# Optimization experiments

Measured on AMD Instinct MI355X. Metric: run time of the kernel, lower is better.

The kernel has to match this reference:

```python
import jax, jax.numpy as jnp
import numpy as np

B, N1, N2, D = 2, 512, 512, 128


def setup_inputs() -> dict:
    key = jax.random.key(0)
    ks = jax.random.split(key, 7)
    return {
        "x0": jax.random.normal(ks[0], (B, N1, D), dtype=jnp.float32),
        "x": jax.random.normal(ks[1], (B, N1, D), dtype=jnp.float32),
        "y": jax.random.normal(ks[2], (B, N2, D), dtype=jnp.float32),
        "W1": jax.random.normal(ks[3], (3 * D, D), dtype=jnp.float32) * (1.0 / np.sqrt(3 * D)),
        "b1": jax.random.normal(ks[4], (D,), dtype=jnp.float32) * 0.02,
        "W2": jax.random.normal(ks[5], (D, 1), dtype=jnp.float32) * (1.0 / np.sqrt(D)),
        "b2": jax.random.normal(ks[6], (1,), dtype=jnp.float32) * 0.02,
    }


def reference(x0, x, y, W1, b1, W2, b2):
    # linear1(concat([x0, x, y], -1)) == x0 @ W1[:D] + x @ W1[D:2D] + y @ W1[2D:] + b1
    d = x.shape[-1]
    Wa, Wb, Wc = W1[:d], W1[d:2 * d], W1[2 * d:]
    # small GEMMs on the un-expanded operands, then broadcast-add over the pair grid
    hx = jnp.einsum('bnd,de->bne', x0, Wa) + jnp.einsum('bnd,de->bne', x, Wb)  # [b, n1, d]
    hy = jnp.einsum('bmd,de->bme', y, Wc)                                      # [b, n2, d]
    h = hx[:, :, None, :] + hy[:, None, :, :] + b1                             # [b, n1, n2, d]
    h = jax.nn.gelu(h, approximate=False)                                      # torch nn.GELU default (erf)
    o = jnp.einsum('bnme,eo->bnmo', h, W2) + b2                                # [b, n1, n2, 1]
    return o[..., 0]                                                           # [b, n1, n2]
```

## Files before the change

kernel.cpp:

```cpp
#include <hip/hip_runtime.h>

#define BB 2
#define NN1 512
#define NN2 512
#define DD 128
#define TS 16
#define SXPAD 132

typedef float v4f __attribute__((ext_vector_type(4)));

struct GeluPoly {
    float p[10];
    constexpr GeluPoly() : p{} {
        const int N = 10;
        const double PI = 3.14159265358979323846;
        double fv[10] = {};
        double xv[10] = {};
        for (int j = 0; j < N; ++j) {
            double th = PI * (j + 0.5) / N;
            double cth = 1.0, term = 1.0, t2 = th * th;
            for (int k = 1; k <= 30; ++k) {
                term *= -t2 / ((2.0 * k - 1.0) * (2.0 * k));
                cth += term;
            }
            xv[j] = cth;
            double t = 4.5 * (cth + 1.0);
            double s = t > 1.0 ? t : 1.0;
            for (int it = 0; it < 64; ++it) s = 0.5 * (s + t / s);
            double x = s * 0.70710678118654752440;
            double esum = 0.0, pw = x, fact = 1.0;
            for (int k = 0; k < 48; ++k) {
                if (k > 0) { fact *= (double)k; pw *= x * x; }
                double tk = pw / (fact * (2.0 * k + 1.0));
                esum += (k & 1) ? -tk : tk;
            }
            double erfv = 1.12837916709551257390 * esum;
            fv[j] = 0.5 * erfv / s;
        }
        double ck[10] = {};
        for (int k = 0; k < N; ++k) {
            double sum = 0.0;
            for (int j = 0; j < N; ++j) {
                double Tk = 1.0;
                if (k >= 1) {
                    double Tm2 = 1.0, Tm1 = xv[j];
                    Tk = xv[j];
                    for (int i = 2; i <= k; ++i) {
                        Tk = 2.0 * xv[j] * Tm1 - Tm2;
                        Tm2 = Tm1; Tm1 = Tk;
                    }
                }
                sum += fv[j] * Tk;
            }
            ck[k] = 2.0 * sum / N;
        }
        ck[0] *= 0.5;
        double T[10][10] = {};
        T[0][0] = 1.0;
        T[1][1] = 1.0;
        for (int k = 2; k < N; ++k)
            for (int i = 0; i < N; ++i)
                T[k][i] = 2.0 * (i > 0 ? T[k - 1][i - 1] : 0.0) - T[k - 2][i];
        double pd[10] = {};
        for (int k = 0; k < N; ++k)
            for (int i = 0; i < N; ++i)
                pd[i] += ck[k] * T[k][i];
        for (int i = 0; i < N; ++i) p[i] = (float)pd[i];
    }
};
static constexpr GeluPoly GP{};

__device__ __forceinline__ float gelu_poly(float s) {
    float c = __builtin_amdgcn_fmed3f(s, -3.0f, 3.0f);
    float t = c * c;
    float u = __builtin_fmaf(t, 0.22222222222222222f, -1.0f);
    float q = GP.p[9];
    #pragma unroll
    for (int k = 8; k >= 0; --k) q = __builtin_fmaf(q, u, GP.p[k]);
    return s * __builtin_fmaf(c, q, 0.5f);
}

#define PR 8
__global__ __launch_bounds__(256) void proj_kernel(
    const float* __restrict__ x0, const float* __restrict__ x,
    const float* __restrict__ y,  const float* __restrict__ W1,
    const float* __restrict__ b1, float* __restrict__ hx, float* __restrict__ hy) {
    const int e = threadIdx.x & (DD - 1);
    const int g = threadIdx.x >> 7;
    const int nxb = (BB * NN1) / PR;
    const float* Wa = W1;
    const float* Wb = W1 + DD * DD;
    const float* Wc = W1 + 2 * DD * DD;

    if (blockIdx.x < nxb) {
        const int row0 = blockIdx.x * PR + g * (PR / 2);
        float acc0 = b1[e], acc1 = b1[e], acc2 = b1[e], acc3 = b1[e];
        #pragma unroll 4
        for (int d = 0; d < DD; ++d) {
            const float wa = Wa[d * DD + e];
            const float wb = Wb[d * DD + e];
            acc0 += x0[(row0 + 0) * DD + d] * wa + x[(row0 + 0) * DD + d] * wb;
            acc1 += x0[(row0 + 1) * DD + d] * wa + x[(row0 + 1) * DD + d] * wb;
            acc2 += x0[(row0 + 2) * DD + d] * wa + x[(row0 + 2) * DD + d] * wb;
            acc3 += x0[(row0 + 3) * DD + d] * wa + x[(row0 + 3) * DD + d] * wb;
        }
        hx[(row0 + 0) * DD + e] = acc0;
        hx[(row0 + 1) * DD + e] = acc1;
        hx[(row0 + 2) * DD + e] = acc2;
        hx[(row0 + 3) * DD + e] = acc3;
    } else {
        const int row0 = (blockIdx.x - nxb) * PR + g * (PR / 2);
        float acc0 = 0.f, acc1 = 0.f, acc2 = 0.f, acc3 = 0.f;
        #pragma unroll 4
        for (int d = 0; d < DD; ++d) {
            const float wc = Wc[d * DD + e];
            acc0 += y[(row0 + 0) * DD + d] * wc;
            acc1 += y[(row0 + 1) * DD + d] * wc;
            acc2 += y[(row0 + 2) * DD + d] * wc;
            acc3 += y[(row0 + 3) * DD + d] * wc;
        }
        hy[(row0 + 0) * DD + e] = acc0;
        hy[(row0 + 1) * DD + e] = acc1;
        hy[(row0 + 2) * DD + e] = acc2;
        hy[(row0 + 3) * DD + e] = acc3;
    }
}

__global__ __launch_bounds__(256) void cross_kernel(
    const float* __restrict__ hx, const float* __restrict__ hy,
    const float* __restrict__ W2, const float* __restrict__ b2,
    float* __restrict__ out) {
    __shared__ float sx[TS][SXPAD];
    __shared__ float sy[TS][SXPAD];
    __shared__ float sw[DD];

    const int b  = blockIdx.z;
    const int n0 = blockIdx.y * TS;
    const int m0 = blockIdx.x * TS;
    const int tid = threadIdx.x;

    for (int i = tid; i < TS * (DD / 4); i += 256) {
        const int r  = i >> 5;
        const int c4 = i & 31;
        *(v4f*)&sx[r][c4 * 4] =
            *(const v4f*)&hx[((b * NN1) + n0 + r) * DD + c4 * 4];
        *(v4f*)&sy[r][c4 * 4] =
            *(const v4f*)&hy[((b * NN2) + m0 + r) * DD + c4 * 4];
    }
    if (tid < DD) sw[tid] = W2[tid];
    __syncthreads();

    const int tn = tid >> 4;
    const int tm = tid & 15;

    float acc = 0.0f;
    #pragma unroll 8
    for (int e4 = 0; e4 < DD / 4; ++e4) {
        const v4f a = *(const v4f*)&sx[tn][e4 * 4];
        const v4f c = *(const v4f*)&sy[tm][e4 * 4];
        const v4f w = *(const v4f*)&sw[e4 * 4];
        acc = __builtin_fmaf(gelu_poly(a.x + c.x), w.x, acc);
        acc = __builtin_fmaf(gelu_poly(a.y + c.y), w.y, acc);
        acc = __builtin_fmaf(gelu_poly(a.z + c.z), w.z, acc);
        acc = __builtin_fmaf(gelu_poly(a.w + c.w), w.w, acc);
    }

    out[((size_t)(b * NN1) + n0 + tn) * NN2 + m0 + tm] = acc + b2[0];
}

extern "C" void kernel_launch(void* const* d_in, const int* in_sizes, int n_in,
                              void* d_out, int out_size, void* d_ws, size_t ws_size,
                              hipStream_t stream) {
    const float* x0 = (const float*)d_in[0];
    const float* x  = (const float*)d_in[1];
    const float* y  = (const float*)d_in[2];
    const float* W1 = (const float*)d_in[3];
    const float* b1 = (const float*)d_in[4];
    const float* W2 = (const float*)d_in[5];
    const float* b2 = (const float*)d_in[6];
    float* out = (float*)d_out;

    float* hx = (float*)d_ws;
    float* hy = hx + (size_t)BB * NN1 * DD;

    const int nblocks = (BB * NN1) / PR + (BB * NN2) / PR;
    proj_kernel<<<nblocks, 256, 0, stream>>>(x0, x, y, W1, b1, hx, hy);
    cross_kernel<<<dim3(NN2 / TS, NN1 / TS, BB), 256, 0, stream>>>(hx, hy, W2, b2, out);
}
```

Baseline: 41.44 us.

## Store hy in interleaved float4 layout and drop LDS tiling in cross kernel

Result: no change. 41.93 us (+1.2%).

```diff
diff --git a/kernel.cpp b/kernel.cpp
--- a/kernel.cpp
+++ b/kernel.cpp
@@ -4,8 +4,6 @@
 #define NN1 512
 #define NN2 512
 #define DD 128
-#define TS 16
-#define SXPAD 132
 
 typedef float v4f __attribute__((ext_vector_type(4)));
 
@@ -84,7 +82,7 @@
 __global__ __launch_bounds__(256) void proj_kernel(
     const float* __restrict__ x0, const float* __restrict__ x,
     const float* __restrict__ y,  const float* __restrict__ W1,
-    const float* __restrict__ b1, float* __restrict__ hx, float* __restrict__ hy) {
+    const float* __restrict__ b1, float* __restrict__ hx, float* __restrict__ hy4) {
     const int e = threadIdx.x & (DD - 1);
     const int g = threadIdx.x >> 7;
     const int nxb = (BB * NN1) / PR;
@@ -110,62 +108,51 @@
         hx[(row0 + 3) * DD + e] = acc3;
     } else {
         const int row0 = (blockIdx.x - nxb) * PR + g * (PR / 2);
-        float acc0 = 0.f, acc1 = 0.f, acc2 = 0.f, acc3 = 0.f;
+        float acc[4];
+        acc[0] = 0.f; acc[1] = 0.f; acc[2] = 0.f; acc[3] = 0.f;
         #pragma unroll 4
         for (int d = 0; d < DD; ++d) {
             const float wc = Wc[d * DD + e];
-            acc0 += y[(row0 + 0) * DD + d] * wc;
-            acc1 += y[(row0 + 1) * DD + d] * wc;
-            acc2 += y[(row0 + 2) * DD + d] * wc;
-            acc3 += y[(row0 + 3) * DD + d] * wc;
+            acc[0] += y[(row0 + 0) * DD + d] * wc;
+            acc[1] += y[(row0 + 1) * DD + d] * wc;
+            acc[2] += y[(row0 + 2) * DD + d] * wc;
+            acc[3] += y[(row0 + 3) * DD + d] * wc;
         }
-        hy[(row0 + 0) * DD + e] = acc0;
-        hy[(row0 + 1) * DD + e] = acc1;
-        hy[(row0 + 2) * DD + e] = acc2;
-        hy[(row0 + 3) * DD + e] = acc3;
+        #pragma unroll
+        for (int i = 0; i < 4; ++i) {
+            const int r = row0 + i;
+            const int bb = r >> 9;
+            const int m = r & (NN2 - 1);
+            hy4[((((size_t)bb * (DD / 4) + (e >> 2)) * NN2) + m) * 4 + (e & 3)] = acc[i];
+        }
     }
 }
 
 __global__ __launch_bounds__(256) void cross_kernel(
-    const float* __restrict__ hx, const float* __restrict__ hy,
+    const float* __restrict__ hx, const float* __restrict__ hy4,
     const float* __restrict__ W2, const float* __restrict__ b2,
     float* __restrict__ out) {
-    __shared__ float sx[TS][SXPAD];
-    __shared__ float sy[TS][SXPAD];
-    __shared__ float sw[DD];
+    const int tid = threadIdx.x;
+    const int b = blockIdx.z;
+    const int n = blockIdx.y;
+    const int m = blockIdx.x * 256 + tid;
 
-    const int b  = blockIdx.z;
-    const int n0 = blockIdx.y * TS;
-    const int m0 = blockIdx.x * TS;
-    const int tid = threadIdx.x;
+    const float* hxrow = hx + ((size_t)b * NN1 + n) * DD;
+    const v4f* hyp = (const v4f*)hy4 + (size_t)b * (DD / 4) * NN2 + m;
 
-    for (int i = tid; i < TS * (DD / 4); i += 256) {
-        const int r  = i >> 5;
-        const int c4 = i & 31;
-        *(v4f*)&sx[r][c4 * 4] =
-            *(const v4f*)&hx[((b * NN1) + n0 + r) * DD + c4 * 4];
-        *(v4f*)&sy[r][c4 * 4] =
-            *(const v4f*)&hy[((b * NN2) + m0 + r) * DD + c4 * 4];
-    }
-    if (tid < DD) sw[tid] = W2[tid];
-    __syncthreads();
-
-    const int tn = tid >> 4;
-    const int tm = tid & 15;
-
-    float acc = 0.0f;
+    float acc = b2[0];
     #pragma unroll 8
     for (int e4 = 0; e4 < DD / 4; ++e4) {
-        const v4f a = *(const v4f*)&sx[tn][e4 * 4];
-        const v4f c = *(const v4f*)&sy[tm][e4 * 4];
-        const v4f w = *(const v4f*)&sw[e4 * 4];
-        acc = __builtin_fmaf(gelu_poly(a.x + c.x), w.x, acc);
-        acc = __builtin_fmaf(gelu_poly(a.y + c.y), w.y, acc);
-        acc = __builtin_fmaf(gelu_poly(a.z + c.z), w.z, acc);
-        acc = __builtin_fmaf(gelu_poly(a.w + c.w), w.w, acc);
+        const v4f hv = hyp[(size_t)e4 * NN2];
+        const v4f ax = *(const v4f*)&hxrow[e4 * 4];
+        const v4f w  = *(const v4f*)&W2[e4 * 4];
+        acc = __builtin_fmaf(gelu_poly(ax.x + hv.x), w.x, acc);
+        acc = __builtin_fmaf(gelu_poly(ax.y + hv.y), w.y, acc);
+        acc = __builtin_fmaf(gelu_poly(ax.z + hv.z), w.z, acc);
+        acc = __builtin_fmaf(gelu_poly(ax.w + hv.w), w.w, acc);
     }
 
-    out[((size_t)(b * NN1) + n0 + tn) * NN2 + m0 + tm] = acc + b2[0];
+    out[((size_t)b * NN1 + n) * NN2 + m] = acc;
 }
 
 extern "C" void kernel_launch(void* const* d_in, const int* in_sizes, int n_in,
@@ -180,10 +167,10 @@
     const float* b2 = (const float*)d_in[6];
     float* out = (float*)d_out;
 
-    float* hx = (float*)d_ws;
-    float* hy = hx + (size_t)BB * NN1 * DD;
+    float* hx  = (float*)d_ws;
+    float* hy4 = hx + (size_t)BB * NN1 * DD;
 
     const int nblocks = (BB * NN1) / PR + (BB * NN2) / PR;
-    proj_kernel<<<nblocks, 256, 0, stream>>>(x0, x, y, W1, b1, hx, hy);
-    cross_kernel<<<dim3(NN2 / TS, NN1 / TS, BB), 256, 0, stream>>>(hx, hy, W2, b2, out);
+    proj_kernel<<<nblocks, 256, 0, stream>>>(x0, x, y, W1, b1, hx, hy4);
+    cross_kernel<<<dim3(NN2 / 256, NN1, BB), 256, 0, stream>>>(hx, hy4, W2, b2, out);
 }
```
